# Kernel tuning notes

Measured on AMD Instinct MI355X. Metric: run time of the kernel, lower is better.

Reference implementation:

```python
import jax, jax.numpy as jnp
import numpy as np
import math

KH, KW, STRIDE, DILATION, Q = 3, 3, 1, 1, 1


def _extract_patches(x, kh, kw, stride, dilation, ph, pw):
    # x: [B, C, H, W] -> patches [B, C, kh*kw, OH*OW], torch.nn.Unfold ordering
    B, C, H, W = x.shape
    xp = jnp.pad(x, ((0, 0), (0, 0), (ph, ph), (pw, pw)))
    oh = (H + 2 * ph - dilation * (kh - 1) - 1) // stride + 1
    ow = (W + 2 * pw - dilation * (kw - 1) - 1) // stride + 1
    slices = []
    for i in range(kh):
        for j in range(kw):
            slices.append(xp[:, :, i * dilation:i * dilation + (oh - 1) * stride + 1:stride,
                              j * dilation:j * dilation + (ow - 1) * stride + 1:stride])
    patches = jnp.stack(slices, axis=2)  # [B, C, kh*kw, OH, OW]
    return patches.reshape(B, C, kh * kw, oh * ow), oh, ow


def setup_inputs() -> dict:
    key = jax.random.key(0)
    k1, k2, k3, k4 = jax.random.split(key, 4)
    B, C, H, W, O = 4, 64, 64, 64, 128
    image = jax.random.normal(k1, (B, C, H, W), dtype=jnp.float32)
    # xavier-like scale for linear weight, then triu on volterra as in reset_parameters
    wl = jax.random.normal(k2, (O, C, KH, KW), dtype=jnp.float32) * 0.02
    wv = jax.random.normal(k3, (O, C, KH * KW, KH * KW), dtype=jnp.float32) * 0.02
    wv = jnp.triu(wv)
    bias = jax.random.uniform(k4, (O,), dtype=jnp.float32, minval=-0.01, maxval=0.01)
    return {"image": image, "weight_linear": wl, "weight_volterra": wv, "bias": bias}


def reference(image, weight_linear, weight_volterra, bias):
    O, C = weight_linear.shape[0], weight_linear.shape[1]
    # q = 1: concat of powers is identity
    ph = int(math.ceil(KH / 2)) - 1
    pw = int(math.ceil(KW / 2)) - 1
    B = image.shape[0]
    patches, oh, ow = _extract_patches(image, KH, KW, STRIDE, DILATION, ph, pw)
    # linear term: [B, O, L]
    kk = KH * KW
    y_lin = jnp.einsum('bckl,ock->bol', patches, weight_linear.reshape(O, C, kk))
    # quadratic Volterra term: per-location outer product xtx [B, L, C, kk, kk]
    p = jnp.transpose(patches, (0, 3, 1, 2))  # [B, L, C, kk]
    xtx = p[..., :, None] * p[..., None, :]   # [B, L, C, kk, kk]
    y_vol = jnp.einsum('blcij,ocij->bol', xtx, weight_volterra)
    out = (y_lin + y_vol).reshape(B, O, oh, ow)
    return out + bias[None, :, None, None]
```

## Files before the change

### kernel.cpp

```cpp
#include <hip/hip_runtime.h>
#include <stdint.h>

typedef __bf16 bf16x8 __attribute__((ext_vector_type(8)));
typedef __bf16 bf16x2 __attribute__((ext_vector_type(2)));
typedef float f32x16 __attribute__((ext_vector_type(16)));

#define CC 64
#define HH 64
#define WW 64
#define OO 128
#define BB 4

__device__ constexpr int TI[25] = {0,0,0,0,0,0,0,0, 1,1,1,1,1,1, 2,2,2,2, 3,3, 0,1,2,3,4};
__device__ constexpr int TJ[25] = {0,1,2,3,4,5,6,7, 1,2,3,4,5,6, 2,3,4,5, 3,4, 8,7,6,5,4};

__device__ __forceinline__ unsigned int pack_bf16(float a, float b) {
#if __has_builtin(__builtin_amdgcn_cvt_pk_bf16_f32)
  bf16x2 r = __builtin_amdgcn_cvt_pk_bf16_f32(a, b);
  return __builtin_bit_cast(unsigned int, r);
#else
  unsigned int ua = __float_as_uint(a) + 0x8000u;
  unsigned int ub = __float_as_uint(b) + 0x8000u;
  return (ua >> 16) | (ub & 0xFFFF0000u);
#endif
}

__device__ float wval(const float* __restrict__ wl, const float* __restrict__ wv,
                      int n, int c, int h, int u) {
  if (u < 7) {
    if (h == 0) return wl[(n * CC + c) * 9 + u];
    int k = 8 - u;
    return (u < 2) ? wl[(n * CC + c) * 9 + k] : 0.f;
  }
  int tt = u - 7;
  int a = TI[tt], bq = TJ[tt];
  if (h == 0) return wv[((n * CC + c) * 9 + a) * 9 + bq];
  if (tt >= 20) return 0.f;
  int a2 = 8 - bq, b2 = 8 - a;
  return wv[((n * CC + c) * 9 + a2) * 9 + b2];
}

__global__ void prep_kernel(const float* __restrict__ wl, const float* __restrict__ wv,
                            unsigned int* __restrict__ Wt) {
  int t = blockIdx.x * 256 + threadIdx.x;
  if (t >= CC * 4 * 4 * 64 * 4) return;
  int ep = t & 3;
  int lane = (t >> 2) & 63;
  int ks = (t >> 8) & 3;
  int ot = (t >> 10) & 3;
  int c = t >> 12;
  int n = ot * 32 + (lane & 31);
  int h = lane >> 5;
  int u0 = ks * 8 + ep * 2;
  float v0 = wval(wl, wv, n, c, h, u0);
  float v1 = wval(wl, wv, n, c, h, u0 + 1);
  Wt[t] = pack_bf16(v0, v1);
}

__global__ __launch_bounds__(1024, 4) void qconv_kernel(
    const float* __restrict__ img, const unsigned int* __restrict__ Wt,
    const float* __restrict__ bias, float* __restrict__ out) {
  __shared__ float red[8][64][16];

  const int t = threadIdx.x;
  const int lane = t & 63;
  const int wq = t >> 6;
  const int ot = wq & 3;
  const int wx = (wq >> 2) & 1;
  const int ch = wq >> 3;
  const int n5 = lane & 31;
  const int h = lane >> 5;
  const int b = blockIdx.x >> 6;
  const int y = blockIdx.x & 63;
  const int x = wx * 32 + n5;

  f32x16 acc;
#pragma unroll
  for (int i = 0; i < 16; ++i) acc[i] = 0.f;

  const int c0 = ch * 32;
  for (int c = c0; c < c0 + 32; ++c) {
    float p[9];
    const float* plane = img + ((b * CC + c) * HH) * WW;
#pragma unroll
    for (int r = 0; r < 3; ++r) {
      int yy = y + r - 1;
      bool okY = (unsigned)yy < 64u;
      const float* rowp = plane + yy * WW;
#pragma unroll
      for (int dx = 0; dx < 3; ++dx) {
        int xx = x + dx - 1;
        float v = 0.f;
        if (okY && (unsigned)xx < 64u) v = rowp[xx];
        p[r * 3 + dx] = v;
      }
    }
    float q[9];
#pragma unroll
    for (int k = 0; k < 9; ++k) q[k] = h ? p[8 - k] : p[k];
    float vals[32];
#pragma unroll
    for (int u = 0; u < 7; ++u) vals[u] = q[u];
#pragma unroll
    for (int tt = 0; tt < 25; ++tt) vals[7 + tt] = q[TI[tt]] * q[TJ[tt]];
    unsigned int pk[16];
#pragma unroll
    for (int i = 0; i < 16; ++i) pk[i] = pack_bf16(vals[2 * i], vals[2 * i + 1]);

    const unsigned int* wbase = Wt + ((c * 4 + ot) * 4) * 256 + lane * 4;
#pragma unroll
    for (int ks = 0; ks < 4; ++ks) {
      uint4 araw = *(const uint4*)(wbase + ks * 256);
      bf16x8 afrag = __builtin_bit_cast(bf16x8, araw);
      uint4 braw = make_uint4(pk[ks * 4], pk[ks * 4 + 1], pk[ks * 4 + 2], pk[ks * 4 + 3]);
      bf16x8 bfrag = __builtin_bit_cast(bf16x8, braw);
      acc = __builtin_amdgcn_mfma_f32_32x32x16_bf16(afrag, bfrag, acc, 0, 0, 0);
    }
  }

  float* redp = &red[ot * 2 + wx][lane][0];
  if (ch == 1) {
#pragma unroll
    for (int r = 0; r < 16; ++r) redp[r] = acc[r];
  }
  __syncthreads();
  if (ch == 0) {
#pragma unroll
    for (int r = 0; r < 16; ++r) {
      int row = (r & 3) + 8 * (r >> 2) + 4 * h;
      int o = ot * 32 + row;
      out[((b * OO + o) * HH + y) * WW + x] = acc[r] + redp[r] + bias[o];
    }
  }
}

extern "C" void kernel_launch(void* const* d_in, const int* in_sizes, int n_in,
                              void* d_out, int out_size, void* d_ws, size_t ws_size,
                              hipStream_t stream) {
  const float* image = (const float*)d_in[0];
  const float* wl = (const float*)d_in[1];
  const float* wv = (const float*)d_in[2];
  const float* bias = (const float*)d_in[3];
  float* out = (float*)d_out;
  unsigned int* Wt = (unsigned int*)d_ws;

  int prep_elems = CC * 4 * 4 * 64 * 4;
  prep_kernel<<<(prep_elems + 255) / 256, 256, 0, stream>>>(wl, wv, Wt);
  qconv_kernel<<<BB * HH, 1024, 0, stream>>>(image, Wt, bias, out);
}
```

Measured before the change: 104.3 us.

## Stage input rows in LDS, tile warps 2x2 over outputs, reduce channels in LDS

Each block now loads its three padded input rows for all channels into shared memory once, instead of every wave gathering its 3x3 patch straight from global memory. The work split changes from 4 output tiles x 2 x-tiles x 2 channel halves to 2 output pairs x 8 channel groups, with each wave computing a 2x2 block of MFMA tiles so A and B fragments are reused. Partial sums from the 8 channel groups are added in LDS one group at a time, with a barrier per step, and then written out as coalesced float4 stores with the bias added. The cost is larger LDS use (about 50 KB), more accumulator registers, and eight serialized reduction phases.

```diff
diff --git a/kernel.cpp b/kernel.cpp
--- a/kernel.cpp
+++ b/kernel.cpp
@@ -57,80 +57,122 @@
   Wt[t] = pack_bf16(v0, v1);
 }
 
-__global__ __launch_bounds__(1024, 4) void qconv_kernel(
+__global__ __launch_bounds__(1024) void qconv_kernel(
     const float* __restrict__ img, const unsigned int* __restrict__ Wt,
     const float* __restrict__ bias, float* __restrict__ out) {
-  __shared__ float red[8][64][16];
+  __shared__ float smem[CC * 3 * 66];
 
   const int t = threadIdx.x;
   const int lane = t & 63;
   const int wq = t >> 6;
-  const int ot = wq & 3;
-  const int wx = (wq >> 2) & 1;
-  const int ch = wq >> 3;
+  const int otp = wq & 1;
+  const int ch = wq >> 1;
   const int n5 = lane & 31;
   const int h = lane >> 5;
   const int b = blockIdx.x >> 6;
   const int y = blockIdx.x & 63;
-  const int x = wx * 32 + n5;
 
-  f32x16 acc;
+  {
+    const int total = CC * 3 * 66;
+    for (int idx = t; idx < total; idx += 1024) {
+      int c = idx / 198;
+      int w = idx - c * 198;
+      int r = w / 66;
+      int s = w - r * 66;
+      int xx = s - 1;
+      int yy = y + r - 1;
+      float v = 0.f;
+      if ((unsigned)xx < 64u && (unsigned)yy < 64u)
+        v = img[((b * CC + c) * HH + yy) * WW + xx];
+      smem[idx] = v;
+    }
+  }
+  __syncthreads();
+
+  f32x16 acc[2][2];
 #pragma unroll
-  for (int i = 0; i < 16; ++i) acc[i] = 0.f;
+  for (int io = 0; io < 2; ++io)
+#pragma unroll
+    for (int xt = 0; xt < 2; ++xt)
+#pragma unroll
+      for (int i = 0; i < 16; ++i) acc[io][xt][i] = 0.f;
 
-  const int c0 = ch * 32;
-  for (int c = c0; c < c0 + 32; ++c) {
-    float p[9];
-    const float* plane = img + ((b * CC + c) * HH) * WW;
+  const int c0 = ch * 8;
+#pragma unroll 1
+  for (int c = c0; c < c0 + 8; ++c) {
+    uint4 bf[2][4];
 #pragma unroll
-    for (int r = 0; r < 3; ++r) {
-      int yy = y + r - 1;
-      bool okY = (unsigned)yy < 64u;
-      const float* rowp = plane + yy * WW;
+    for (int xt = 0; xt < 2; ++xt) {
+      const int xb = xt * 32 + n5;
+      float pv[9];
 #pragma unroll
-      for (int dx = 0; dx < 3; ++dx) {
-        int xx = x + dx - 1;
-        float v = 0.f;
-        if (okY && (unsigned)xx < 64u) v = rowp[xx];
-        p[r * 3 + dx] = v;
+      for (int r = 0; r < 3; ++r)
+#pragma unroll
+        for (int d = 0; d < 3; ++d)
+          pv[r * 3 + d] = smem[(c * 3 + r) * 66 + xb + d];
+      float q[9];
+#pragma unroll
+      for (int k = 0; k < 9; ++k) q[k] = h ? pv[8 - k] : pv[k];
+      unsigned int pk[16];
+#pragma unroll
+      for (int i = 0; i < 16; ++i) {
+        const int u0 = 2 * i, u1 = 2 * i + 1;
+        float v0 = (u0 < 7) ? q[u0] : q[TI[u0 - 7]] * q[TJ[u0 - 7]];
+        float v1 = (u1 < 7) ? q[u1] : q[TI[u1 - 7]] * q[TJ[u1 - 7]];
+        pk[i] = pack_bf16(v0, v1);
       }
+#pragma unroll
+      for (int ks = 0; ks < 4; ++ks)
+        bf[xt][ks] = make_uint4(pk[4 * ks], pk[4 * ks + 1], pk[4 * ks + 2], pk[4 * ks + 3]);
     }
-    float q[9];
-#pragma unroll
-    for (int k = 0; k < 9; ++k) q[k] = h ? p[8 - k] : p[k];
-    float vals[32];
-#pragma unroll
-    for (int u = 0; u < 7; ++u) vals[u] = q[u];
-#pragma unroll
-    for (int tt = 0; tt < 25; ++tt) vals[7 + tt] = q[TI[tt]] * q[TJ[tt]];
-    unsigned int pk[16];
-#pragma unroll
-    for (int i = 0; i < 16; ++i) pk[i] = pack_bf16(vals[2 * i], vals[2 * i + 1]);
 
-    const unsigned int* wbase = Wt + ((c * 4 + ot) * 4) * 256 + lane * 4;
+    const unsigned int* wb = Wt + (c * 16 + otp * 8) * 256 + lane * 4;
 #pragma unroll
     for (int ks = 0; ks < 4; ++ks) {
-      uint4 araw = *(const uint4*)(wbase + ks * 256);
-      bf16x8 afrag = __builtin_bit_cast(bf16x8, araw);
-      uint4 braw = make_uint4(pk[ks * 4], pk[ks * 4 + 1], pk[ks * 4 + 2], pk[ks * 4 + 3]);
-      bf16x8 bfrag = __builtin_bit_cast(bf16x8, braw);
-      acc = __builtin_amdgcn_mfma_f32_32x32x16_bf16(afrag, bfrag, acc, 0, 0, 0);
+#pragma unroll
+      for (int io = 0; io < 2; ++io) {
+        uint4 araw = *(const uint4*)(wb + (io * 4 + ks) * 256);
+        bf16x8 af = __builtin_bit_cast(bf16x8, araw);
+        acc[io][0] = __builtin_amdgcn_mfma_f32_32x32x16_bf16(
+            af, __builtin_bit_cast(bf16x8, bf[0][ks]), acc[io][0], 0, 0, 0);
+        acc[io][1] = __builtin_amdgcn_mfma_f32_32x32x16_bf16(
+            af, __builtin_bit_cast(bf16x8, bf[1][ks]), acc[io][1], 0, 0, 0);
+      }
     }
   }
 
-  float* redp = &red[ot * 2 + wx][lane][0];
-  if (ch == 1) {
+  __syncthreads();
+  float* out_s = smem;
+#pragma unroll 1
+  for (int rr = 0; rr < 8; ++rr) {
+    if (ch == rr) {
 #pragma unroll
-    for (int r = 0; r < 16; ++r) redp[r] = acc[r];
+      for (int io = 0; io < 2; ++io)
+#pragma unroll
+        for (int xt = 0; xt < 2; ++xt)
+#pragma unroll
+          for (int r = 0; r < 16; ++r) {
+            int o = (otp * 2 + io) * 32 + (r & 3) + 8 * (r >> 2) + 4 * h;
+            int x = xt * 32 + n5;
+            float v = acc[io][xt][r];
+            if (rr == 0) out_s[o * 64 + x] = v;
+            else out_s[o * 64 + x] += v;
+          }
+    }
+    __syncthreads();
   }
-  __syncthreads();
-  if (ch == 0) {
-#pragma unroll
-    for (int r = 0; r < 16; ++r) {
-      int row = (r & 3) + 8 * (r >> 2) + 4 * h;
-      int o = ot * 32 + row;
-      out[((b * OO + o) * HH + y) * WW + x] = acc[r] + redp[r] + bias[o];
-    }
+
+  {
+    int o = t >> 3;
+    int x0 = (t & 7) * 8;
+    float bo = bias[o];
+    float4 v0 = *(const float4*)&out_s[o * 64 + x0];
+    float4 v1 = *(const float4*)&out_s[o * 64 + x0 + 4];
+    v0.x += bo; v0.y += bo; v0.z += bo; v0.w += bo;
+    v1.x += bo; v1.y += bo; v1.z += bo; v1.w += bo;
+    float* op = out + ((b * OO + o) * HH + y) * WW + x0;
+    *(float4*)op = v0;
+    *(float4*)(op + 4) = v1;
   }
 }
 
```

Result: slower. 125.7 us (+20.6%).
